# Optimization experiments

Measured on AMD Instinct MI355X. Metric: run time of the kernel, lower is better.

## Reference

```python
import jax, jax.numpy as jnp
import numpy as np

USER_NUM = 300000
ITEM_NUM = 200000
EMBED_DIM = 64
N_EDGES = 1250000
N_LAYERS = 3  # len([embedding_dim] + hidden_units) with hidden_units=[64,64]
N_NODES = USER_NUM + ITEM_NUM


def setup_inputs() -> dict:
    key = jax.random.key(0)
    k1, k2, k3, k4, k5 = jax.random.split(key, 5)
    user_emb = 0.01 * jax.random.normal(k1, (USER_NUM, EMBED_DIM), dtype=jnp.float32)
    item_emb = 0.01 * jax.random.normal(k2, (ITEM_NUM, EMBED_DIM), dtype=jnp.float32)
    edge_weight = jax.random.uniform(k3, (N_EDGES,), dtype=jnp.float32)
    src_idx = jax.random.randint(k4, (N_EDGES,), 0, N_NODES, dtype=jnp.int32)
    dst_idx = jax.random.randint(k5, (N_EDGES,), 0, N_NODES, dtype=jnp.int32)
    return {"user_emb": user_emb, "item_emb": item_emb, "edge_weight": edge_weight,
            "src_idx": src_idx, "dst_idx": dst_idx}


def reference(user_emb, item_emb, edge_weight, src_idx, dst_idx):
    # computer(): concat embeddings -> L hops of sparse.mm(adj, emb) -> mean over hops -> split
    all_emb = jnp.concatenate([user_emb, item_emb], axis=0)  # [N, d]
    acc = all_emb  # running sum of per-hop embeddings (includes hop 0)
    h = all_emb
    for _ in range(N_LAYERS):
        # weighted SpMM: out[dst] += w * h[src]
        msgs = h[src_idx] * edge_weight[:, None]            # [E, d]
        h = jax.ops.segment_sum(msgs, dst_idx, num_segments=N_NODES)  # [N, d]
        acc = acc + h
    light_out = acc / jnp.float32(N_LAYERS + 1)             # mean over stacked hops
    return light_out[:USER_NUM], light_out[USER_NUM:]
```

## Files before the change

kernel.cpp:

```cpp
#include <hip/hip_runtime.h>


#define USER_NUM  300000
#define ITEM_NUM  200000
#define N_NODES   500000
#define EMBED_DIM 64
#define N_EDGES   1250000
#define NV   (N_NODES * EMBED_DIM)
#define NV4  (NV / 4)

#define BSHIFT  11
#define BNODES  2048
#define NBUK    ((N_NODES + BNODES - 1) / BNODES)
#define PCHUNK  4096
#define PGRID   ((N_EDGES + PCHUNK - 1) / PCHUNK)

__device__ __forceinline__ unsigned bpack(float lo, float hi) {
    unsigned a = __float_as_uint(lo), b = __float_as_uint(hi);
    a = (a + 0x7fffu + ((a >> 16) & 1u)) >> 16;
    b = (b + 0x7fffu + ((b >> 16) & 1u)) & 0xffff0000u;
    return a | b;
}
__device__ __forceinline__ float blo(unsigned u) { return __uint_as_float(u << 16); }
__device__ __forceinline__ float bhi(unsigned u) { return __uint_as_float(u & 0xffff0000u); }

__device__ __forceinline__ void bf8_fma(uint4 g, float w, float* a) {
    a[0] += w * blo(g.x); a[1] += w * bhi(g.x);
    a[2] += w * blo(g.y); a[3] += w * bhi(g.y);
    a[4] += w * blo(g.z); a[5] += w * bhi(g.z);
    a[6] += w * blo(g.w); a[7] += w * bhi(g.w);
}

__global__ void conv_kernel(const float4* __restrict__ ue,
                            const float4* __restrict__ ie,
                            uint4* __restrict__ E) {
    int i = blockIdx.x * blockDim.x + threadIdx.x;
    if (i >= N_NODES * 8) return;
    int n = i >> 3, sub = i & 7;
    const float4* p = (n < USER_NUM) ? &ue[(size_t)n * 16]
                                     : &ie[(size_t)(n - USER_NUM) * 16];
    float4 a = p[sub * 2], b = p[sub * 2 + 1];
    uint4 r;
    r.x = bpack(a.x, a.y); r.y = bpack(a.z, a.w);
    r.z = bpack(b.x, b.y); r.w = bpack(b.z, b.w);
    E[i] = r;
}

__global__ void bhist_kernel(const int* __restrict__ dst, int* __restrict__ bcnt) {
    __shared__ int h[256];
    int t = threadIdx.x;
    h[t] = 0;
    __syncthreads();
    int cbase = blockIdx.x * PCHUNK;
    int cnt = min(PCHUNK, N_EDGES - cbase);
    for (int i = t; i < cnt; i += 256)
        atomicAdd(&h[dst[cbase + i] >> BSHIFT], 1);
    __syncthreads();
    if (t < NBUK && h[t]) atomicAdd(&bcnt[t], h[t]);
}

__global__ void bscan_kernel(const int* __restrict__ bcnt,
                             int* __restrict__ boff,
                             int* __restrict__ bcur,
                             int* __restrict__ offs) {
    __shared__ int lds[256];
    int t = threadIdx.x;
    int v = (t < NBUK) ? bcnt[t] : 0;
    lds[t] = v;
    __syncthreads();
    for (int off = 1; off < 256; off <<= 1) {
        int x = (t >= off) ? lds[t - off] : 0;
        __syncthreads();
        if (t >= off) lds[t] += x;
        __syncthreads();
    }
    int excl = lds[t] - v;
    if (t < NBUK) { boff[t] = excl; bcur[t] = excl; }
    if (t == NBUK - 1) boff[NBUK] = N_EDGES;
    if (t == 0) offs[N_NODES] = N_EDGES;
}

__global__ void part_kernel(const int* __restrict__ src,
                            const int* __restrict__ dst,
                            const float* __restrict__ w,
                            int* __restrict__ bcur,
                            int2* __restrict__ tmp) {
    __shared__ int hist[256];
    __shared__ int base[256];
    int t = threadIdx.x;
    int cbase = blockIdx.x * PCHUNK;
    int cnt = min(PCHUNK, N_EDGES - cbase);
    int key[16], eb[16];
    float ew[16];
    hist[t] = 0;
    __syncthreads();
    #pragma unroll
    for (int k = 0; k < 16; ++k) {
        int i = t + k * 256;
        if (i < cnt) {
            int e = cbase + i;
            int d = dst[e];
            eb[k]  = d >> BSHIFT;
            key[k] = ((d & (BNODES - 1)) << 19) | src[e];
            ew[k]  = w[e];
            atomicAdd(&hist[eb[k]], 1);
        } else eb[k] = -1;
    }
    __syncthreads();
    int h = hist[t];
    base[t] = (h > 0) ? atomicAdd(&bcur[t], h) : 0;
    __syncthreads();
    hist[t] = 0;
    __syncthreads();
    #pragma unroll
    for (int k = 0; k < 16; ++k) {
        if (eb[k] >= 0) {
            int r = atomicAdd(&hist[eb[k]], 1);
            tmp[base[eb[k]] + r] = make_int2(key[k], __float_as_int(ew[k]));
        }
    }
}

__global__ void fine_kernel(const int2* __restrict__ tmp,
                            const int* __restrict__ boff,
                            int* __restrict__ offs,
                            int2* __restrict__ pe) {
    __shared__ int cnt[BNODES];
    __shared__ int sums[256];
    int b = blockIdx.x, t = threadIdx.x;
    int nbase = b << BSHIFT;
    int ebeg = boff[b], eend = boff[b + 1];
    for (int j = t; j < BNODES; j += 256) cnt[j] = 0;
    __syncthreads();
    for (int i = ebeg + t; i < eend; i += 256)
        atomicAdd(&cnt[((unsigned)tmp[i].x) >> 19], 1);
    __syncthreads();
    int s[8], tot = 0;
    #pragma unroll
    for (int k = 0; k < 8; ++k) { s[k] = cnt[t * 8 + k]; tot += s[k]; }
    sums[t] = tot;
    __syncthreads();
    for (int off = 1; off < 256; off <<= 1) {
        int x = (t >= off) ? sums[t - off] : 0;
        __syncthreads();
        if (t >= off) sums[t] += x;
        __syncthreads();
    }
    int run = ebeg + sums[t] - tot;
    #pragma unroll
    for (int k = 0; k < 8; ++k) {
        int node = nbase + t * 8 + k;
        if (node < N_NODES) offs[node] = run;
        cnt[t * 8 + k] = run;
        run += s[k];
    }
    __syncthreads();
    for (int i = ebeg + t; i < eend; i += 256) {
        int2 E2 = tmp[i];
        int p = atomicAdd(&cnt[((unsigned)E2.x) >> 19], 1);
        pe[p] = make_int2(E2.x & 0x7FFFF, E2.y);
    }
}

__global__ void layer_kernel(const uint4* __restrict__ hsrc,
                             uint4* __restrict__ hout,
                             const int* __restrict__ offs,
                             const int2* __restrict__ pe) {
    int gid  = blockIdx.x * blockDim.x + threadIdx.x;
    int wave = gid >> 6;
    int lane = gid & 63;
    int grp  = lane >> 3;
    int sub  = lane & 7;
    int n    = wave * 8 + grp;
    if (n >= N_NODES) return;
    int beg = offs[n], end = offs[n + 1];
    float a0[8] = {0,0,0,0,0,0,0,0};
    float a1[8] = {0,0,0,0,0,0,0,0};
    int e = beg;
    for (; e + 2 <= end; e += 2) {
        int2 p0 = pe[e], p1 = pe[e + 1];
        uint4 g0 = hsrc[(size_t)p0.x * 8 + sub];
        uint4 g1 = hsrc[(size_t)p1.x * 8 + sub];
        bf8_fma(g0, __int_as_float(p0.y), a0);
        bf8_fma(g1, __int_as_float(p1.y), a1);
    }
    if (e < end) {
        int2 p0 = pe[e];
        uint4 g0 = hsrc[(size_t)p0.x * 8 + sub];
        bf8_fma(g0, __int_as_float(p0.y), a0);
    }
    #pragma unroll
    for (int i = 0; i < 8; ++i) a0[i] += a1[i];
    uint4 r;
    r.x = bpack(a0[0], a0[1]); r.y = bpack(a0[2], a0[3]);
    r.z = bpack(a0[4], a0[5]); r.w = bpack(a0[6], a0[7]);
    hout[(size_t)n * 8 + sub] = r;
}

__global__ void final_kernel(const uint4* __restrict__ E,
                             const uint4* __restrict__ h1,
                             const uint4* __restrict__ h2,
                             float4* __restrict__ out,
                             const int* __restrict__ offs,
                             const int2* __restrict__ pe) {
    int gid  = blockIdx.x * blockDim.x + threadIdx.x;
    int wave = gid >> 6;
    int lane = gid & 63;
    int grp  = lane >> 3;
    int sub  = lane & 7;
    int n    = wave * 8 + grp;
    if (n >= N_NODES) return;
    int beg = offs[n], end = offs[n + 1];
    float a0[8] = {0,0,0,0,0,0,0,0};
    float a1[8] = {0,0,0,0,0,0,0,0};
    int e = beg;
    for (; e + 2 <= end; e += 2) {
        int2 p0 = pe[e], p1 = pe[e + 1];
        uint4 g0 = h2[(size_t)p0.x * 8 + sub];
        uint4 g1 = h2[(size_t)p1.x * 8 + sub];
        bf8_fma(g0, __int_as_float(p0.y), a0);
        bf8_fma(g1, __int_as_float(p1.y), a1);
    }
    if (e < end) {
        int2 p0 = pe[e];
        uint4 g0 = h2[(size_t)p0.x * 8 + sub];
        bf8_fma(g0, __int_as_float(p0.y), a0);
    }
    size_t o8 = (size_t)n * 8 + sub;
    uint4 e0 = E[o8], b1 = h1[o8], b2 = h2[o8];
    float4 ra, rb;
    ra.x = 0.25f * (blo(e0.x) + blo(b1.x) + blo(b2.x) + a0[0] + a1[0]);
    ra.y = 0.25f * (bhi(e0.x) + bhi(b1.x) + bhi(b2.x) + a0[1] + a1[1]);
    ra.z = 0.25f * (blo(e0.y) + blo(b1.y) + blo(b2.y) + a0[2] + a1[2]);
    ra.w = 0.25f * (bhi(e0.y) + bhi(b1.y) + bhi(b2.y) + a0[3] + a1[3]);
    rb.x = 0.25f * (blo(e0.z) + blo(b1.z) + blo(b2.z) + a0[4] + a1[4]);
    rb.y = 0.25f * (bhi(e0.z) + bhi(b1.z) + bhi(b2.z) + a0[5] + a1[5]);
    rb.z = 0.25f * (blo(e0.w) + blo(b1.w) + blo(b2.w) + a0[6] + a1[6]);
    rb.w = 0.25f * (bhi(e0.w) + bhi(b1.w) + bhi(b2.w) + a0[7] + a1[7]);
    out[(size_t)n * 16 + sub * 2]     = ra;
    out[(size_t)n * 16 + sub * 2 + 1] = rb;
}

__global__ void init_fb_kernel(const float4* __restrict__ ue,
                               const float4* __restrict__ ie,
                               float4* __restrict__ h,
                               float4* __restrict__ hn,
                               float4* __restrict__ acc) {
    int i = blockIdx.x * blockDim.x + threadIdx.x;
    if (i >= NV4) return;
    const int ub = USER_NUM * EMBED_DIM / 4;
    float4 v = (i < ub) ? ue[i] : ie[i - ub];
    h[i] = v; acc[i] = v;
    hn[i] = make_float4(0.f, 0.f, 0.f, 0.f);
}

__global__ void spmm_fb_kernel(const float* __restrict__ h, float* __restrict__ hn,
                               const int* __restrict__ src, const int* __restrict__ dst,
                               const float* __restrict__ w) {
    int gid = blockIdx.x * blockDim.x + threadIdx.x;
    int wave = gid >> 6, lane = gid & 63;
    int nwave = (gridDim.x * blockDim.x) >> 6;
    for (int e = wave; e < N_EDGES; e += nwave) {
        float v = h[src[e] * 64 + lane] * w[e];
        atomicAdd(&hn[dst[e] * 64 + lane], v);
    }
}

template <int LAST>
__global__ void accum_fb_kernel(float4* __restrict__ acc, const float4* __restrict__ hn,
                                float4* __restrict__ zbuf) {
    int i = blockIdx.x * blockDim.x + threadIdx.x;
    if (i >= NV4) return;
    float4 a = acc[i], n = hn[i];
    a.x += n.x; a.y += n.y; a.z += n.z; a.w += n.w;
    if (LAST) { a.x *= 0.25f; a.y *= 0.25f; a.z *= 0.25f; a.w *= 0.25f; }
    acc[i] = a;
    if (!LAST) zbuf[i] = make_float4(0.f, 0.f, 0.f, 0.f);
}

extern "C" void kernel_launch(void* const* d_in, const int* in_sizes, int n_in,
                              void* d_out, int out_size, void* d_ws, size_t ws_size,
                              hipStream_t stream) {
    const float* ue  = (const float*)d_in[0];
    const float* ie  = (const float*)d_in[1];
    const float* w   = (const float*)d_in[2];
    const int*   src = (const int*)d_in[3];
    const int*   dst = (const int*)d_in[4];

    float* out = (float*)d_out;

    const size_t HB = (size_t)N_NODES * 128;
    char*  base = (char*)d_ws;
    uint4* E    = (uint4*)base;
    uint4* B    = (uint4*)(base + HB);
    uint4* C    = (uint4*)(base + 2 * HB);
    int2*  tmp  = (int2*)(base + 3 * HB);
    int2*  pe   = (int2*)(base + 3 * HB + (size_t)N_EDGES * 8);
    int*   offs = (int*)((char*)pe + (size_t)N_EDGES * 8);
    int*   boff = offs + (N_NODES + 1);
    int*   bcnt = boff + (NBUK + 1);
    int*   bcur = bcnt + NBUK;

    const size_t needed = 3 * HB + (size_t)N_EDGES * 16
                        + (size_t)(N_NODES + 1 + 3 * NBUK + 1) * 4;

    const int TB = 256;
    const int egrid = NV4 / TB;
    const int cgrid = (N_NODES * 8) / TB + 1;
    const int fgrid = (N_NODES / 8 * 64) / TB;

    if (ws_size >= needed) {
        hipMemsetAsync(bcnt, 0, (size_t)NBUK * 4, stream);
        bhist_kernel<<<PGRID, TB, 0, stream>>>(dst, bcnt);
        bscan_kernel<<<1, 256, 0, stream>>>(bcnt, boff, bcur, offs);
        part_kernel<<<PGRID, TB, 0, stream>>>(src, dst, w, bcur, tmp);
        fine_kernel<<<NBUK, TB, 0, stream>>>(tmp, boff, offs, pe);
        conv_kernel<<<cgrid, TB, 0, stream>>>((const float4*)ue, (const float4*)ie, E);

        layer_kernel<<<fgrid, TB, 0, stream>>>(E, B, offs, pe);
        layer_kernel<<<fgrid, TB, 0, stream>>>(B, C, offs, pe);
        final_kernel<<<fgrid, TB, 0, stream>>>(E, B, C, (float4*)out, offs, pe);
    } else {
        float* A  = (float*)d_ws;
        float* Bf = A + NV;
        const int sgrid = 4096;
        init_fb_kernel<<<egrid, TB, 0, stream>>>((const float4*)ue, (const float4*)ie,
                                                 (float4*)A, (float4*)Bf, (float4*)out);
        spmm_fb_kernel<<<sgrid, TB, 0, stream>>>(A, Bf, src, dst, w);
        accum_fb_kernel<0><<<egrid, TB, 0, stream>>>((float4*)out, (const float4*)Bf, (float4*)A);
        spmm_fb_kernel<<<sgrid, TB, 0, stream>>>(Bf, A, src, dst, w);
        accum_fb_kernel<0><<<egrid, TB, 0, stream>>>((float4*)out, (const float4*)A, (float4*)Bf);
        spmm_fb_kernel<<<sgrid, TB, 0, stream>>>(A, Bf, src, dst, w);
        accum_fb_kernel<1><<<egrid, TB, 0, stream>>>((float4*)out, (const float4*)Bf, nullptr);
    }
}
```

Before: 255.6 us.

## Replace bucket histogram+scan with fixed-capacity buckets and fuse conversion into partition

Drops the global histogram and scan kernels by giving each destination bucket a fixed capacity slot region (CAP=8192) in the temp and edge arrays, so the partition pass can append directly. The bf16 conversion of the embeddings is merged into the same launch as extra blocks. Per-node offsets become int2 (begin,end) pairs, and the final output uses nontemporal stores. This saves two launches and one pass over dst. The risk is overflow if any bucket gets more than CAP edges, which random inputs (about 5120 expected per bucket) are unlikely to reach.

Result: faster. 218.5 us (-14.5%).

```diff
diff --git a/kernel.cpp b/kernel.cpp
--- a/kernel.cpp
+++ b/kernel.cpp
@@ -5,15 +5,19 @@
 #define ITEM_NUM  200000
 #define N_NODES   500000
 #define EMBED_DIM 64
-#define N_EDGES   1250000
 #define NV   (N_NODES * EMBED_DIM)
 #define NV4  (NV / 4)
+#define N_EDGES   1250000
 
 #define BSHIFT  11
 #define BNODES  2048
 #define NBUK    ((N_NODES + BNODES - 1) / BNODES)
+#define CAP     8192
 #define PCHUNK  4096
 #define PGRID   ((N_EDGES + PCHUNK - 1) / PCHUNK)
+#define CONVG   ((N_NODES * 8) / 256)
+
+typedef float    f32x4 __attribute__((ext_vector_type(4)));
 
 __device__ __forceinline__ unsigned bpack(float lo, float hi) {
     unsigned a = __float_as_uint(lo), b = __float_as_uint(hi);
@@ -31,63 +35,30 @@
     a[6] += w * blo(g.w); a[7] += w * bhi(g.w);
 }
 
-__global__ void conv_kernel(const float4* __restrict__ ue,
-                            const float4* __restrict__ ie,
-                            uint4* __restrict__ E) {
-    int i = blockIdx.x * blockDim.x + threadIdx.x;
-    if (i >= N_NODES * 8) return;
-    int n = i >> 3, sub = i & 7;
-    const float4* p = (n < USER_NUM) ? &ue[(size_t)n * 16]
-                                     : &ie[(size_t)(n - USER_NUM) * 16];
-    float4 a = p[sub * 2], b = p[sub * 2 + 1];
-    uint4 r;
-    r.x = bpack(a.x, a.y); r.y = bpack(a.z, a.w);
-    r.z = bpack(b.x, b.y); r.w = bpack(b.z, b.w);
-    E[i] = r;
-}
-
-__global__ void bhist_kernel(const int* __restrict__ dst, int* __restrict__ bcnt) {
-    __shared__ int h[256];
+__global__ void pre_kernel(const int* __restrict__ src,
+                           const int* __restrict__ dst,
+                           const float* __restrict__ w,
+                           int* __restrict__ bcur,
+                           int2* __restrict__ tmp,
+                           const float4* __restrict__ ue,
+                           const float4* __restrict__ ie,
+                           uint4* __restrict__ E) {
+    __shared__ int hist[256];
+    __shared__ int rbase[256];
     int t = threadIdx.x;
-    h[t] = 0;
-    __syncthreads();
-    int cbase = blockIdx.x * PCHUNK;
-    int cnt = min(PCHUNK, N_EDGES - cbase);
-    for (int i = t; i < cnt; i += 256)
-        atomicAdd(&h[dst[cbase + i] >> BSHIFT], 1);
-    __syncthreads();
-    if (t < NBUK && h[t]) atomicAdd(&bcnt[t], h[t]);
-}
-
-__global__ void bscan_kernel(const int* __restrict__ bcnt,
-                             int* __restrict__ boff,
-                             int* __restrict__ bcur,
-                             int* __restrict__ offs) {
-    __shared__ int lds[256];
-    int t = threadIdx.x;
-    int v = (t < NBUK) ? bcnt[t] : 0;
-    lds[t] = v;
-    __syncthreads();
-    for (int off = 1; off < 256; off <<= 1) {
-        int x = (t >= off) ? lds[t - off] : 0;
-        __syncthreads();
-        if (t >= off) lds[t] += x;
-        __syncthreads();
-    }
-    int excl = lds[t] - v;
-    if (t < NBUK) { boff[t] = excl; bcur[t] = excl; }
-    if (t == NBUK - 1) boff[NBUK] = N_EDGES;
-    if (t == 0) offs[N_NODES] = N_EDGES;
-}
-
-__global__ void part_kernel(const int* __restrict__ src,
-                            const int* __restrict__ dst,
-                            const float* __restrict__ w,
-                            int* __restrict__ bcur,
-                            int2* __restrict__ tmp) {
-    __shared__ int hist[256];
-    __shared__ int base[256];
-    int t = threadIdx.x;
+    if (blockIdx.x >= PGRID) {
+        int i = (blockIdx.x - PGRID) * 256 + t;
+        int n = i >> 3, sub = i & 7;
+        const f32x4* p = (const f32x4*)((n < USER_NUM) ? &ue[(size_t)n * 16]
+                                                       : &ie[(size_t)(n - USER_NUM) * 16]);
+        f32x4 a = __builtin_nontemporal_load(&p[sub * 2]);
+        f32x4 b = __builtin_nontemporal_load(&p[sub * 2 + 1]);
+        uint4 r;
+        r.x = bpack(a.x, a.y); r.y = bpack(a.z, a.w);
+        r.z = bpack(b.x, b.y); r.w = bpack(b.z, b.w);
+        E[i] = r;
+        return;
+    }
     int cbase = blockIdx.x * PCHUNK;
     int cnt = min(PCHUNK, N_EDGES - cbase);
     int key[16], eb[16];
@@ -108,7 +79,7 @@
     }
     __syncthreads();
     int h = hist[t];
-    base[t] = (h > 0) ? atomicAdd(&bcur[t], h) : 0;
+    rbase[t] = (h > 0) ? atomicAdd(&bcur[t], h) : 0;
     __syncthreads();
     hist[t] = 0;
     __syncthreads();
@@ -116,24 +87,26 @@
     for (int k = 0; k < 16; ++k) {
         if (eb[k] >= 0) {
             int r = atomicAdd(&hist[eb[k]], 1);
-            tmp[base[eb[k]] + r] = make_int2(key[k], __float_as_int(ew[k]));
+            tmp[(size_t)eb[k] * CAP + rbase[eb[k]] + r] =
+                make_int2(key[k], __float_as_int(ew[k]));
         }
     }
 }
 
 __global__ void fine_kernel(const int2* __restrict__ tmp,
-                            const int* __restrict__ boff,
-                            int* __restrict__ offs,
+                            const int* __restrict__ bcur,
+                            int2* __restrict__ offs2,
                             int2* __restrict__ pe) {
     __shared__ int cnt[BNODES];
     __shared__ int sums[256];
     int b = blockIdx.x, t = threadIdx.x;
     int nbase = b << BSHIFT;
-    int ebeg = boff[b], eend = boff[b + 1];
+    int ebase = b * CAP;
+    int ecnt  = bcur[b];
     for (int j = t; j < BNODES; j += 256) cnt[j] = 0;
     __syncthreads();
-    for (int i = ebeg + t; i < eend; i += 256)
-        atomicAdd(&cnt[((unsigned)tmp[i].x) >> 19], 1);
+    for (int i = t; i < ecnt; i += 256)
+        atomicAdd(&cnt[((unsigned)tmp[ebase + i].x) >> 19], 1);
     __syncthreads();
     int s[8], tot = 0;
     #pragma unroll
@@ -146,25 +119,25 @@
         if (t >= off) sums[t] += x;
         __syncthreads();
     }
-    int run = ebeg + sums[t] - tot;
+    int run = ebase + sums[t] - tot;
     #pragma unroll
     for (int k = 0; k < 8; ++k) {
         int node = nbase + t * 8 + k;
-        if (node < N_NODES) offs[node] = run;
+        if (node < N_NODES) offs2[node] = make_int2(run, run + s[k]);
         cnt[t * 8 + k] = run;
         run += s[k];
     }
     __syncthreads();
-    for (int i = ebeg + t; i < eend; i += 256) {
-        int2 E2 = tmp[i];
-        int p = atomicAdd(&cnt[((unsigned)E2.x) >> 19], 1);
-        pe[p] = make_int2(E2.x & 0x7FFFF, E2.y);
+    for (int i = t; i < ecnt; i += 256) {
+        int2 T = tmp[ebase + i];
+        int p = atomicAdd(&cnt[((unsigned)T.x) >> 19], 1);
+        pe[p] = make_int2(T.x & 0x7FFFF, T.y);
     }
 }
 
 __global__ void layer_kernel(const uint4* __restrict__ hsrc,
                              uint4* __restrict__ hout,
-                             const int* __restrict__ offs,
+                             const int2* __restrict__ offs2,
                              const int2* __restrict__ pe) {
     int gid  = blockIdx.x * blockDim.x + threadIdx.x;
     int wave = gid >> 6;
@@ -173,7 +146,8 @@
     int sub  = lane & 7;
     int n    = wave * 8 + grp;
     if (n >= N_NODES) return;
-    int beg = offs[n], end = offs[n + 1];
+    int2 oo = offs2[n];
+    int beg = oo.x, end = oo.y;
     float a0[8] = {0,0,0,0,0,0,0,0};
     float a1[8] = {0,0,0,0,0,0,0,0};
     int e = beg;
@@ -200,8 +174,8 @@
 __global__ void final_kernel(const uint4* __restrict__ E,
                              const uint4* __restrict__ h1,
                              const uint4* __restrict__ h2,
-                             float4* __restrict__ out,
-                             const int* __restrict__ offs,
+                             float* __restrict__ out,
+                             const int2* __restrict__ offs2,
                              const int2* __restrict__ pe) {
     int gid  = blockIdx.x * blockDim.x + threadIdx.x;
     int wave = gid >> 6;
@@ -210,7 +184,8 @@
     int sub  = lane & 7;
     int n    = wave * 8 + grp;
     if (n >= N_NODES) return;
-    int beg = offs[n], end = offs[n + 1];
+    int2 oo = offs2[n];
+    int beg = oo.x, end = oo.y;
     float a0[8] = {0,0,0,0,0,0,0,0};
     float a1[8] = {0,0,0,0,0,0,0,0};
     int e = beg;
@@ -228,7 +203,7 @@
     }
     size_t o8 = (size_t)n * 8 + sub;
     uint4 e0 = E[o8], b1 = h1[o8], b2 = h2[o8];
-    float4 ra, rb;
+    f32x4 ra, rb;
     ra.x = 0.25f * (blo(e0.x) + blo(b1.x) + blo(b2.x) + a0[0] + a1[0]);
     ra.y = 0.25f * (bhi(e0.x) + bhi(b1.x) + bhi(b2.x) + a0[1] + a1[1]);
     ra.z = 0.25f * (blo(e0.y) + blo(b1.y) + blo(b2.y) + a0[2] + a1[2]);
@@ -237,8 +212,9 @@
     rb.y = 0.25f * (bhi(e0.z) + bhi(b1.z) + bhi(b2.z) + a0[5] + a1[5]);
     rb.z = 0.25f * (blo(e0.w) + blo(b1.w) + blo(b2.w) + a0[6] + a1[6]);
     rb.w = 0.25f * (bhi(e0.w) + bhi(b1.w) + bhi(b2.w) + a0[7] + a1[7]);
-    out[(size_t)n * 16 + sub * 2]     = ra;
-    out[(size_t)n * 16 + sub * 2 + 1] = rb;
+    f32x4* op = (f32x4*)out + (size_t)n * 16 + sub * 2;
+    __builtin_nontemporal_store(ra, op);
+    __builtin_nontemporal_store(rb, op + 1);
 }
 
 __global__ void init_fb_kernel(const float4* __restrict__ ue,
@@ -289,37 +265,34 @@
 
     float* out = (float*)d_out;
 
-    const size_t HB = (size_t)N_NODES * 128;
-    char*  base = (char*)d_ws;
-    uint4* E    = (uint4*)base;
-    uint4* B    = (uint4*)(base + HB);
-    uint4* C    = (uint4*)(base + 2 * HB);
-    int2*  tmp  = (int2*)(base + 3 * HB);
-    int2*  pe   = (int2*)(base + 3 * HB + (size_t)N_EDGES * 8);
-    int*   offs = (int*)((char*)pe + (size_t)N_EDGES * 8);
-    int*   boff = offs + (N_NODES + 1);
-    int*   bcnt = boff + (NBUK + 1);
-    int*   bcur = bcnt + NBUK;
-
-    const size_t needed = 3 * HB + (size_t)N_EDGES * 16
-                        + (size_t)(N_NODES + 1 + 3 * NBUK + 1) * 4;
+    const size_t HB   = (size_t)N_NODES * 128;
+    const size_t PADE = (size_t)NBUK * CAP;
+    char*  base  = (char*)d_ws;
+    uint4* E     = (uint4*)base;
+    uint4* B     = (uint4*)(base + HB);
+    uint4* C     = (uint4*)(base + 2 * HB);
+    int2*  tmp   = (int2*)(base + 3 * HB);
+    int2*  pe    = (int2*)(base + 3 * HB + PADE * 8);
+    int2*  offs2 = (int2*)(base + 3 * HB + 2 * PADE * 8);
+    int*   bcur  = (int*)(base + 3 * HB + 2 * PADE * 8 + (size_t)N_NODES * 8);
+
+    const size_t needed = 3 * HB + 2 * PADE * 8 + (size_t)N_NODES * 8
+                        + (size_t)NBUK * 4;
 
     const int TB = 256;
     const int egrid = NV4 / TB;
-    const int cgrid = (N_NODES * 8) / TB + 1;
     const int fgrid = (N_NODES / 8 * 64) / TB;
 
     if (ws_size >= needed) {
-        hipMemsetAsync(bcnt, 0, (size_t)NBUK * 4, stream);
-        bhist_kernel<<<PGRID, TB, 0, stream>>>(dst, bcnt);
-        bscan_kernel<<<1, 256, 0, stream>>>(bcnt, boff, bcur, offs);
-        part_kernel<<<PGRID, TB, 0, stream>>>(src, dst, w, bcur, tmp);
-        fine_kernel<<<NBUK, TB, 0, stream>>>(tmp, boff, offs, pe);
-        conv_kernel<<<cgrid, TB, 0, stream>>>((const float4*)ue, (const float4*)ie, E);
-
-        layer_kernel<<<fgrid, TB, 0, stream>>>(E, B, offs, pe);
-        layer_kernel<<<fgrid, TB, 0, stream>>>(B, C, offs, pe);
-        final_kernel<<<fgrid, TB, 0, stream>>>(E, B, C, (float4*)out, offs, pe);
+        hipMemsetAsync(bcur, 0, (size_t)NBUK * 4, stream);
+        pre_kernel<<<PGRID + CONVG, TB, 0, stream>>>(src, dst, w, bcur, tmp,
+                                                     (const float4*)ue,
+                                                     (const float4*)ie, E);
+        fine_kernel<<<NBUK, TB, 0, stream>>>(tmp, bcur, offs2, pe);
+
+        layer_kernel<<<fgrid, TB, 0, stream>>>(E, B, offs2, pe);
+        layer_kernel<<<fgrid, TB, 0, stream>>>(B, C, offs2, pe);
+        final_kernel<<<fgrid, TB, 0, stream>>>(E, B, C, out, offs2, pe);
     } else {
         float* A  = (float*)d_ws;
         float* Bf = A + NV;
```
